# Performance work log

Hardware: AMD Instinct MI355X
Metric: run time of the kernel (lower is better)

Reference implementation:

```python
import jax, jax.numpy as jnp
import numpy as np

B, S, E = 4, 2048, 1024
H = 4
DH = E // H          # 256 head dim
DQ = E // 4          # 256 quaternion d_model
ALPHA = 1.5
EPS = 1e-10
FOCUS = 0.9
SEL = 2.0


def setup_inputs() -> dict:
    key = jax.random.key(0)
    ks = jax.random.split(key, 6)
    sc = 0.02
    return {
        "x": jax.random.normal(ks[0], (B, S, E), dtype=jnp.float32),
        "in_proj_w": jax.random.normal(ks[1], (3 * E, E), dtype=jnp.float32) * sc,
        "in_proj_b": jnp.zeros((3 * E,), dtype=jnp.float32),
        "out_w": jax.random.normal(ks[2], (E, E), dtype=jnp.float32) * sc,
        "out_b": jnp.zeros((E,), dtype=jnp.float32),
        "m_w1": jax.random.normal(ks[3], (E, E), dtype=jnp.float32) * sc,
        "m_b1": jnp.zeros((E,), dtype=jnp.float32),
        "m_w2": jax.random.normal(ks[4], (E, E), dtype=jnp.float32) * sc,
        "m_b2": jnp.zeros((E,), dtype=jnp.float32),
    }


def quaternion_multiply(q1, q2):
    # Hamilton product over last dim of size 4 (complex-valued components).
    w1, x1, y1, z1 = q1[..., 0], q1[..., 1], q1[..., 2], q1[..., 3]
    w2, x2, y2, z2 = q2[..., 0], q2[..., 1], q2[..., 2], q2[..., 3]
    return jnp.stack([
        w1 * w2 - x1 * x2 - y1 * y2 - z1 * z2,
        w1 * x2 + x1 * w2 + y1 * z2 - z1 * y2,
        w1 * y2 - x1 * z2 + y1 * w2 + z1 * x2,
        w1 * z2 + x1 * y2 - y1 * x2 + z1 * w2,
    ], axis=-1)


def _mha(x, in_proj_w, in_proj_b, out_w, out_b):
    # torch nn.MultiheadAttention self-attention, batch_first
    qkv = x @ in_proj_w.T + in_proj_b              # [B,S,3E]
    q, k, v = jnp.split(qkv, 3, axis=-1)
    q = q.reshape(B, S, H, DH)
    k = k.reshape(B, S, H, DH)
    v = v.reshape(B, S, H, DH)
    scores = jnp.einsum('bqhd,bkhd->bhqk', q, k) / jnp.sqrt(jnp.float32(DH))
    attn = jax.nn.softmax(scores, axis=-1)
    out = jnp.einsum('bhqk,bkhd->bqhd', attn, v).reshape(B, S, E)
    return out @ out_w.T + out_b


def _spectral_attention(signal):
    sq = signal.reshape(B, S, DQ, 4)
    sfft = jnp.fft.fft(sq, axis=-3)                 # complex64, FFT over seq
    kk = jnp.arange(S, dtype=jnp.float32)
    filt = jnp.exp(1j * ALPHA * jnp.arctan(jnp.log(kk + EPS)))  # [S] complex
    sf = sfft * filt[None, :, None, None]
    inter = quaternion_multiply(quaternion_multiply(sf, sf), sf)
    attended = jnp.fft.ifft(inter, axis=-3).real
    return attended.reshape(B, S, E)


def reference(x, in_proj_w, in_proj_b, out_w, out_b, m_w1, m_b1, m_w2, m_b2):
    nicotinic = _mha(x, in_proj_w, in_proj_b, out_w, out_b)
    h = jax.nn.gelu(x @ m_w1.T + m_b1, approximate=False)
    muscarinic = h @ m_w2.T + m_b2
    chol = FOCUS * nicotinic + (1.0 - FOCUS) * muscarinic
    attn_w = _spectral_attention(chol * SEL)
    return x * attn_w
```

## Files before the change

kernel.cpp:

```cpp
#include <hip/hip_runtime.h>
#include <cstdint>

typedef _Float16 f16;
typedef unsigned short u16;
typedef __attribute__((ext_vector_type(8))) _Float16 half8;
typedef __attribute__((ext_vector_type(4))) _Float16 half4;
typedef __attribute__((ext_vector_type(2))) __fp16 fp16x2;
typedef __attribute__((ext_vector_type(4))) float f32x4;

#define MFMA_F16(a, b, c) __builtin_amdgcn_mfma_f32_16x16x32_f16(a, b, c, 0, 0, 0)

#define WAITVM8() asm volatile("s_waitcnt vmcnt(8)" ::: "memory")
#define WAITVM4() asm volatile("s_waitcnt vmcnt(4)" ::: "memory")
#define WAITVM2() asm volatile("s_waitcnt vmcnt(2)" ::: "memory")
#define WAITVM0() asm volatile("s_waitcnt vmcnt(0)" ::: "memory")
#define BARRIER() do { asm volatile("" ::: "memory"); __builtin_amdgcn_s_barrier(); \
                       asm volatile("" ::: "memory"); } while (0)

__device__ inline void stage16(const void* g, void* l) {
#if defined(__has_builtin) && __has_builtin(__builtin_amdgcn_global_load_lds)
  __builtin_amdgcn_global_load_lds(
      (const __attribute__((address_space(1))) unsigned*)g,
      (__attribute__((address_space(3))) unsigned*)l, 16, 0, 0);
#else
  *(int4*)l = *(const int4*)g;
#endif
}

__device__ inline int pack_f16(float a, float b) {
#if defined(__has_builtin) && __has_builtin(__builtin_amdgcn_cvt_pkrtz)
  union { fp16x2 h; int i; } u;
  u.h = __builtin_amdgcn_cvt_pkrtz(a, b);
  return u.i;
#else
  union { f16 h[2]; int i; } u;
  u.h[0] = (f16)a; u.h[1] = (f16)b;
  return u.i;
#endif
}

__global__ __launch_bounds__(256)
void conv_all(const float* __restrict__ x, const float* __restrict__ wqkv,
              const float* __restrict__ w1, const float* __restrict__ wout,
              const float* __restrict__ w2, f16* __restrict__ dst) {
  int i = (blockIdx.x * 256 + threadIdx.x) * 8;
  const float* src; size_t dofs; float sc = 1.0f;
  if (i < 8388608)       { src = x + i;               dofs = i; }
  else if (i < 11534336) { src = wqkv + (i - 8388608); dofs = i; }
  else if (i < 12582912) { src = w1 + (i - 11534336);  dofs = i; }
  else if (i < 13631488) {
    int t = i - 12582912; int j = t >> 10, k = t & 1023;
    src = wout + t; dofs = 12582912 + (size_t)j * 2048 + k; sc = 1.8f;
  } else {
    int t = i - 13631488; int j = t >> 10, k = t & 1023;
    src = w2 + t; dofs = 12582912 + (size_t)j * 2048 + 1024 + k; sc = 0.2f;
  }
  float4 a = *(const float4*)src;
  float4 b = *(const float4*)(src + 4);
  half8 h;
  h[0] = (f16)(a.x * sc); h[1] = (f16)(a.y * sc); h[2] = (f16)(a.z * sc); h[3] = (f16)(a.w * sc);
  h[4] = (f16)(b.x * sc); h[5] = (f16)(b.y * sc); h[6] = (f16)(b.z * sc); h[7] = (f16)(b.w * sc);
  *(half8*)(dst + dofs) = h;
}

__global__ __launch_bounds__(256)
void filt_init(float2* __restrict__ ftab) {
  int k = blockIdx.x * 256 + threadIdx.x;
  if (k < 2048) {
    float s, c;
    sincosf(1.5f * atanf(logf((float)k + 1e-10f)), &s, &c);
    ftab[k] = make_float2(c, s);
  }
}

template<int EPI>
__global__ __launch_bounds__(256, 2)
void gemm_f16(const f16* __restrict__ A, const f16* __restrict__ W,
              const float* __restrict__ bias0, const float* __restrict__ bias1,
              void* __restrict__ out0, void* __restrict__ out1,
              f16* __restrict__ Vt, int N, int K) {
  __shared__ __align__(16) f16 lds[2][16384];
  const int tid = threadIdx.x;
  const int lane = tid & 63, w = tid >> 6;
  const int g = lane >> 4, lm = lane & 15;
  const int wr = w >> 1, wc = w & 1;
  const int nwg = gridDim.x * gridDim.y;
  const int flat = blockIdx.y * gridDim.x + blockIdx.x;
  const int logical = (flat & 7) * (nwg >> 3) + (flat >> 3);
  const int bx = logical % gridDim.x, by = logical / gridDim.x;
  const int m0 = by * 128, n0 = bx * 128;

  const f16* src[8];
#pragma unroll
  for (int j = 0; j < 8; ++j) {
    int u = j * 256 + tid;
    if (u < 1024) {
      int row = u >> 3, s = u & 7;
      src[j] = A + (size_t)(m0 + row) * K + ((s ^ (row & 7)) << 3);
    } else {
      int v = u - 1024;
      int row = v >> 3, s = v & 7;
      src[j] = W + (size_t)(n0 + row) * K + ((s ^ (row & 7)) << 3);
    }
  }

  f32x4 acc[4][4];
#pragma unroll
  for (int mt = 0; mt < 4; ++mt)
#pragma unroll
    for (int nt = 0; nt < 4; ++nt) acc[mt][nt] = (f32x4){0.f, 0.f, 0.f, 0.f};

#pragma unroll
  for (int j = 0; j < 8; ++j) stage16(src[j], &lds[0][(j * 256 + tid) * 8]);
  __syncthreads();

  const int KT = K >> 6;
#pragma unroll 1
  for (int t = 0; t < KT; ++t) {
    const f16* bufA = lds[t & 1];
    const f16* bufB = bufA + 8192;
    if (t + 1 < KT) {
#pragma unroll
      for (int j = 0; j < 8; ++j) {
        src[j] += 64;
        stage16(src[j], &lds[(t + 1) & 1][(j * 256 + tid) * 8]);
      }
      WAITVM8();
    } else {
      WAITVM0();
    }
    BARRIER();
#pragma unroll
    for (int ks = 0; ks < 2; ++ks) {
      half8 a[4], b[4];
#pragma unroll
      for (int mt = 0; mt < 4; ++mt) {
        int row = wr * 64 + mt * 16 + lm;
        a[mt] = *(const half8*)(bufA + row * 64 + (((ks * 4 + g) ^ (row & 7)) << 3));
      }
#pragma unroll
      for (int nt = 0; nt < 4; ++nt) {
        int row = wc * 64 + nt * 16 + lm;
        b[nt] = *(const half8*)(bufB + row * 64 + (((ks * 4 + g) ^ (row & 7)) << 3));
      }
#pragma unroll
      for (int mt = 0; mt < 4; ++mt)
#pragma unroll
        for (int nt = 0; nt < 4; ++nt)
          acc[mt][nt] = MFMA_F16(a[mt], b[nt], acc[mt][nt]);
    }
    BARRIER();
  }

  const int crow = m0 + wr * 64 + g * 4;
  const int ccol = n0 + wc * 64 + lm;
  if (EPI == 3) {
    if (n0 < 2048) {
      f16* qk = (f16*)out0;
#pragma unroll
      for (int nt = 0; nt < 4; ++nt) {
        float bb = bias0[ccol + nt * 16];
#pragma unroll
        for (int mt = 0; mt < 4; ++mt)
#pragma unroll
          for (int r = 0; r < 4; ++r)
            qk[(size_t)(crow + mt * 16 + r) * 3072 + ccol + nt * 16] =
                (f16)(acc[mt][nt][r] + bb);
      }
    } else if (n0 < 3072) {
      f16* ldsT = (f16*)lds;
#pragma unroll
      for (int nt = 0; nt < 4; ++nt) {
        float bb = bias0[ccol + nt * 16];
        int c = wc * 64 + nt * 16 + lm;
#pragma unroll
        for (int mt = 0; mt < 4; ++mt) {
          int r = wr * 64 + mt * 16 + g * 4;
#pragma unroll
          for (int rr = 0; rr < 4; ++rr)
            ldsT[c * 136 + r + rr] = (f16)(acc[mt][nt][rr] + bb);
        }
      }
      BARRIER();
      const int vbase0 = n0 - 2048;
      const int b = m0 >> 11, srow = m0 & 2047;
#pragma unroll
      for (int it = 0; it < 8; ++it) {
        int id = it * 256 + tid;
        int c = id >> 4, rb = id & 15;
        int vcol = vbase0 + c;
        int h = vcol >> 8, d = vcol & 255;
        half8 v = *(half8*)&ldsT[c * 136 + rb * 8];
        *(half8*)&Vt[(((size_t)(b * 4 + h)) * 256 + d) * 2048 + srow + rb * 8] = v;
      }
    } else {
      f16* cat = (f16*)out1;
      const int hc = ccol - 3072;
#pragma unroll
      for (int nt = 0; nt < 4; ++nt) {
        float bb = bias1[hc + nt * 16];
#pragma unroll
        for (int mt = 0; mt < 4; ++mt)
#pragma unroll
          for (int r = 0; r < 4; ++r) {
            float v = acc[mt][nt][r] + bb;
            v = 0.5f * v * (1.0f + erff(v * 0.70710678118654752f));
            cat[(size_t)(crow + mt * 16 + r) * 2048 + 1024 + hc + nt * 16] = (f16)v;
          }
      }
    }
  } else {
    f16* ldsT = (f16*)lds;
#pragma unroll
    for (int nt = 0; nt < 4; ++nt) {
      float bb = 1.8f * bias0[ccol + nt * 16] + 0.2f * bias1[ccol + nt * 16];
      int c = wc * 64 + nt * 16 + lm;
#pragma unroll
      for (int mt = 0; mt < 4; ++mt) {
        int r = wr * 64 + mt * 16 + g * 4;
#pragma unroll
        for (int rr = 0; rr < 4; ++rr)
          ldsT[c * 136 + r + rr] = (f16)(acc[mt][nt][rr] + bb);
      }
    }
    BARRIER();
    f16* ch = (f16*)out0;
#pragma unroll
    for (int it = 0; it < 8; ++it) {
      int id = it * 256 + tid;
      int c = id >> 4, rb = id & 15;
      half8 v = *(half8*)&ldsT[c * 136 + rb * 8];
      *(half8*)&ch[(size_t)(n0 + c) * 8192 + m0 + rb * 8] = v;
    }
  }
}

__global__ __launch_bounds__(512, 2)
void flash_f16(const f16* __restrict__ qkv, const f16* __restrict__ Vt,
               f16* __restrict__ attn) {
  __shared__ __align__(16) f16 lds[32768];
  const int tid = threadIdx.x;
  const int lane = tid & 63, w = tid >> 6;
  const int g = lane >> 4, lm = lane & 15;
  const int raw = blockIdx.x;
  const int bh = (raw & 7) * 2 + (raw >> 7);
  const int qt = (raw >> 3) & 15;
  const int b = bh >> 2, h = bh & 3;
  const int q0 = qt * 128 + w * 16;
  const float SC = 0.09016844005555896f;

  half8 qf[8];
  {
    const f16* qp = qkv + (size_t)(b * 2048 + q0 + lm) * 3072 + h * 256 + g * 8;
#pragma unroll
    for (int c = 0; c < 8; ++c) qf[c] = *(const half8*)(qp + c * 32);
  }

  const f16* kbase = qkv + (size_t)b * 2048 * 3072 + 1024 + h * 256;
  const f16* vbase = Vt + (size_t)bh * 256 * 2048;
  int kofs[2], vofs[2];
#pragma unroll
  for (int j = 0; j < 2; ++j) {
    int u = j * 512 + tid;
    int kv = u >> 5, s = u & 31;
    kofs[j] = kv * 3072 + ((s ^ (kv & 7)) << 3);
    int d = u >> 2, sl = u & 3;
    vofs[j] = d * 2048 + ((sl ^ ((d >> 1) & 3)) << 3);
  }

  f32x4 o[16];
#pragma unroll
  for (int f = 0; f < 16; ++f) o[f] = (f32x4){0.f, 0.f, 0.f, 0.f};
  float m = -3e38f, l = 0.f;
  half8 paP = (half8){0, 0, 0, 0, 0, 0, 0, 0};

#pragma unroll
  for (int j = 0; j < 2; ++j) stage16(kbase + kofs[j], &lds[(j * 512 + tid) * 8]);

#pragma unroll 1
  for (int t = 0; t < 64; ++t) {
    const int cb_ = t & 1;
    if (t < 63) {
      const int kt = (t + 1) * 98304;
#pragma unroll
      for (int j = 0; j < 2; ++j)
        stage16(kbase + kofs[j] + kt, &lds[(cb_ ^ 1) * 8192 + (j * 512 + tid) * 8]);
    }
    {
      const int vt_ = t * 32;
#pragma unroll
      for (int j = 0; j < 2; ++j)
        stage16(vbase + vofs[j] + vt_, &lds[16384 + cb_ * 8192 + (j * 512 + tid) * 8]);
    }
    if (t < 63) { WAITVM4(); } else { WAITVM2(); }
    BARRIER();

    const f16* kb = &lds[cb_ * 8192];

    f32x4 s0 = {0.f, 0.f, 0.f, 0.f}, s1 = {0.f, 0.f, 0.f, 0.f};
    __builtin_amdgcn_s_setprio(1);
#pragma unroll
    for (int c = 0; c < 8; ++c) {
      int slot = ((c * 4 + g) ^ (lm & 7)) << 3;
      half8 b0 = *(const half8*)(kb + lm * 256 + slot);
      half8 b1 = *(const half8*)(kb + (16 + lm) * 256 + slot);
      s0 = MFMA_F16(b0, qf[c], s0);
      s1 = MFMA_F16(b1, qf[c], s1);
    }
    __builtin_amdgcn_s_setprio(0);

    if (t > 0) {
      const f16* vbp = &lds[16384 + (cb_ ^ 1) * 8192];
      __builtin_amdgcn_s_setprio(1);
#pragma unroll
      for (int f = 0; f < 16; ++f) {
        int d = f * 16 + lm;
        half8 bv = *(const half8*)(vbp + d * 32 + ((g ^ ((d >> 1) & 3)) << 3));
        o[f] = MFMA_F16(paP, bv, o[f]);
      }
      __builtin_amdgcn_s_setprio(0);
    }

    float a0[4], a1[4];
#pragma unroll
    for (int r = 0; r < 4; ++r) { a0[r] = s0[r] * SC; a1[r] = s1[r] * SC; }
    float mx = fmaxf(fmaxf(fmaxf(a0[0], a0[1]), fmaxf(a0[2], a0[3])),
                     fmaxf(fmaxf(a1[0], a1[1]), fmaxf(a1[2], a1[3])));
    mx = fmaxf(mx, __shfl_xor(mx, 16));
    mx = fmaxf(mx, __shfl_xor(mx, 32));

    if (!__all(mx <= m + 8.0f)) {
      float mn = fmaxf(m, mx);
      float corr = exp2f(m - mn);
      m = mn; l *= corr;
#pragma unroll
      for (int r = 0; r < 4; ++r) {
        float cr = __shfl(corr, ((lane >> 2) & 12) + r);
#pragma unroll
        for (int f = 0; f < 16; ++f) o[f][r] *= cr;
      }
    }

    float e0[4], e1[4], rs;
#pragma unroll
    for (int r = 0; r < 4; ++r) { e0[r] = exp2f(a0[r] - m); e1[r] = exp2f(a1[r] - m); }
    rs = ((e0[0] + e0[1]) + (e0[2] + e0[3])) + ((e1[0] + e1[1]) + (e1[2] + e1[3]));
    rs += __shfl_xor(rs, 16);
    rs += __shfl_xor(rs, 32);
    l += rs;

    int A01 = pack_f16(e0[0], e0[1]);
    int A23 = pack_f16(e0[2], e0[3]);
    int B01 = pack_f16(e1[0], e1[1]);
    int B23 = pack_f16(e1[2], e1[3]);
    const int s1l = ((lane & 16) << 1) + lm;
    const int s2l = s1l + 16;
    int t0a = __shfl(A01, s1l), t0b = __shfl(B01, s1l);
    int t1a = __shfl(A23, s1l), t1b = __shfl(B23, s1l);
    int t2a = __shfl(A01, s2l), t2b = __shfl(B01, s2l);
    int t3a = __shfl(A23, s2l), t3b = __shfl(B23, s2l);
    union { int i[4]; half8 h; } pau;
    const bool hi = lane >= 32;
    pau.i[0] = hi ? t0b : t0a;
    pau.i[1] = hi ? t1b : t1a;
    pau.i[2] = hi ? t2b : t2a;
    pau.i[3] = hi ? t3b : t3a;
    paP = pau.h;

    BARRIER();
  }

  WAITVM0();
  BARRIER();
  {
    const f16* vbp = &lds[16384 + 8192];
#pragma unroll
    for (int f = 0; f < 16; ++f) {
      int d = f * 16 + lm;
      half8 bv = *(const half8*)(vbp + d * 32 + ((g ^ ((d >> 1) & 3)) << 3));
      o[f] = MFMA_F16(paP, bv, o[f]);
    }
  }

  float inv[4];
#pragma unroll
  for (int r = 0; r < 4; ++r) inv[r] = 1.0f / __shfl(l, ((lane >> 2) & 12) + r);
#pragma unroll
  for (int f = 0; f < 16; ++f)
#pragma unroll
    for (int r = 0; r < 4; ++r)
      attn[(size_t)(b * 2048 + q0 + g * 4 + r) * 2048 + h * 256 + f * 16 + lm] =
          (f16)(o[f][r] * inv[r]);
}

__device__ inline float2 cmul(float2 a, float2 b) {
  return make_float2(a.x * b.x - a.y * b.y, a.x * b.y + a.y * b.x);
}
__device__ inline float2 cmulc(float2 a, float2 b) {
  return make_float2(a.x * b.x + a.y * b.y, a.y * b.x - a.x * b.y);
}
__device__ inline void qcube(float2& w, float2& x, float2& y, float2& z, float2 f) {
  w = cmul(w, f); x = cmul(x, f); y = cmul(y, f); z = cmul(z, f);
  float2 a2 = cmul(w, w);
  float2 sx = cmul(x, x), sy = cmul(y, y), sz = cmul(z, z);
  float2 s = make_float2(sx.x + sy.x + sz.x, sx.y + sy.y + sz.y);
  float2 t3 = make_float2(a2.x - 3.f * s.x, a2.y - 3.f * s.y);
  float2 cf = make_float2(3.f * a2.x - s.x, 3.f * a2.y - s.y);
  w = cmul(w, t3); x = cmul(cf, x); y = cmul(cf, y); z = cmul(cf, z);
}

__device__ inline int fftpos(int k) {
  int kp = k >> 1;
  return ((k & 1) << 10) | ((kp & 3) << 8) | ((kp & 12) << 4) | (kp & 48)
       | ((kp >> 4) & 12) | ((kp >> 8) & 3);
}

__global__ __launch_bounds__(256)
void spectral6(const f16* __restrict__ cholT, const float* __restrict__ xin,
               const float2* __restrict__ ftab, float* __restrict__ outp) {
  __shared__ __align__(16) float2 Z[2][2048];
  __shared__ float2 tw[1024];
  const int tid = threadIdx.x;
  const int b = blockIdx.x >> 8;
  const int qd = blockIdx.x & 255;
  const size_t c0 = (size_t)qd * 4;
  const f16* t0 = cholT + (c0 + 0) * 8192 + b * 2048;
  const f16* t1 = cholT + (c0 + 1) * 8192 + b * 2048;
  const f16* t2 = cholT + (c0 + 2) * 8192 + b * 2048;
  const f16* t3 = cholT + (c0 + 3) * 8192 + b * 2048;

  for (int j = tid; j < 1024; j += 256) {
    float ang = -6.2831853071795864769f * (float)j * (1.0f / 2048.0f);
    float sv, cv; sincosf(ang, &sv, &cv);
    tw[j] = make_float2(cv, sv);
  }
  for (int s = tid; s < 1024; s += 256) {
    float2 z0a = make_float2((float)t0[s], (float)t1[s]);
    float2 z1a = make_float2((float)t2[s], (float)t3[s]);
    float2 z0b = make_float2((float)t0[s + 1024], (float)t1[s + 1024]);
    float2 z1b = make_float2((float)t2[s + 1024], (float)t3[s + 1024]);
    float2 w = tw[s];
    Z[0][s] = make_float2(z0a.x + z0b.x, z0a.y + z0b.y);
    Z[0][s + 1024] = cmul(make_float2(z0a.x - z0b.x, z0a.y - z0b.y), w);
    Z[1][s] = make_float2(z1a.x + z1b.x, z1a.y + z1b.y);
    Z[1][s + 1024] = cmul(make_float2(z1a.x - z1b.x, z1a.y - z1b.y), w);
  }
  __syncthreads();

#pragma unroll 1
  for (int lq = 8; lq >= 0; lq -= 2) {
    const int Q = 1 << lq, st = 512 >> lq;
#pragma unroll 1
    for (int it = 0; it < 4; ++it) {
      int gg = it * 256 + tid;
      int c = gg >> 9, bf = gg & 511;
      int j = bf & (Q - 1);
      int base = ((bf >> lq) << (lq + 2)) | j;
      float2 a = Z[c][base], bq = Z[c][base + Q];
      float2 cc = Z[c][base + 2 * Q], d = Z[c][base + 3 * Q];
      float2 t0_ = make_float2(a.x + cc.x, a.y + cc.y);
      float2 t1_ = make_float2(a.x - cc.x, a.y - cc.y);
      float2 t2_ = make_float2(bq.x + d.x, bq.y + d.y);
      float2 bd = make_float2(bq.x - d.x, bq.y - d.y);
      float2 t3_ = make_float2(bd.y, -bd.x);
      float2 y0 = make_float2(t0_.x + t2_.x, t0_.y + t2_.y);
      float2 y1 = make_float2(t1_.x + t3_.x, t1_.y + t3_.y);
      float2 y2 = make_float2(t0_.x - t2_.x, t0_.y - t2_.y);
      float2 y3 = make_float2(t1_.x - t3_.x, t1_.y - t3_.y);
      int i3 = 3 * j * st;
      float sg = (i3 & 1024) ? -1.f : 1.f;
      i3 &= 1023;
      Z[c][base] = y0;
      Z[c][base + Q] = cmul(y1, tw[j * st]);
      Z[c][base + 2 * Q] = cmul(y2, tw[2 * j * st]);
      float2 r3 = cmul(y3, tw[i3]);
      Z[c][base + 3 * Q] = make_float2(r3.x * sg, r3.y * sg);
    }
    __syncthreads();
  }

#pragma unroll 1
  for (int it = 0; it < 4; ++it) {
    int jj = it * 256 + tid;
    int nrep = (jj == 0) ? 2 : 1;
#pragma unroll 1
    for (int rep = 0; rep < nrep; ++rep) {
      int k  = (jj == 0) ? (rep ? 1024 : 0) : jj;
      int kn = (jj == 0) ? k : 2048 - jj;
      int p  = fftpos(k);
      int pp = fftpos(kn);
      float2 z0p = Z[0][p], z0q = Z[0][pp];
      float2 z1p = Z[1][p], z1q = Z[1][pp];
      float2 wk = make_float2(0.5f * (z0p.x + z0q.x), 0.5f * (z0p.y - z0q.y));
      float2 xk = make_float2(0.5f * (z0p.y + z0q.y), 0.5f * (z0q.x - z0p.x));
      float2 yk = make_float2(0.5f * (z1p.x + z1q.x), 0.5f * (z1p.y - z1q.y));
      float2 zk = make_float2(0.5f * (z1p.y + z1q.y), 0.5f * (z1q.x - z1p.x));
      float2 wn = make_float2(0.5f * (z0q.x + z0p.x), 0.5f * (z0q.y - z0p.y));
      float2 xn = make_float2(0.5f * (z0q.y + z0p.y), 0.5f * (z0p.x - z0q.x));
      float2 yn = make_float2(0.5f * (z1q.x + z1p.x), 0.5f * (z1q.y - z1p.y));
      float2 zn = make_float2(0.5f * (z1q.y + z1p.y), 0.5f * (z1p.x - z1q.x));
      float2 fk = ftab[k], fn = ftab[kn];
      qcube(wk, xk, yk, zk, fk);
      qcube(wn, xn, yn, zn, fn);
      Z[0][p]  = make_float2(0.5f * (wk.x + wn.x) - 0.5f * (xk.y - xn.y),
                             0.5f * (wk.y - wn.y) + 0.5f * (xk.x + xn.x));
      Z[0][pp] = make_float2(0.5f * (wn.x + wk.x) - 0.5f * (xn.y - xk.y),
                             0.5f * (wn.y - wk.y) + 0.5f * (xn.x + xk.x));
      Z[1][p]  = make_float2(0.5f * (yk.x + yn.x) - 0.5f * (zk.y - zn.y),
                             0.5f * (yk.y - yn.y) + 0.5f * (zk.x + zn.x));
      Z[1][pp] = make_float2(0.5f * (yn.x + yk.x) - 0.5f * (zn.y - zk.y),
                             0.5f * (yn.y - yk.y) + 0.5f * (zn.x + zk.x));
    }
  }
  __syncthreads();

#pragma unroll 1
  for (int lq = 0; lq <= 8; lq += 2) {
    const int Q = 1 << lq, st = 512 >> lq;
#pragma unroll 1
    for (int it = 0; it < 4; ++it) {
      int gg = it * 256 + tid;
      int c = gg >> 9, bf = gg & 511;
      int j = bf & (Q - 1);
      int base = ((bf >> lq) << (lq + 2)) | j;
      float2 a = Z[c][base];
      float2 bq = cmulc(Z[c][base + Q], tw[j * st]);
      float2 cc = cmulc(Z[c][base + 2 * Q], tw[2 * j * st]);
      int i3 = 3 * j * st;
      float sg = (i3 & 1024) ? -1.f : 1.f;
      i3 &= 1023;
      float2 d = cmulc(Z[c][base + 3 * Q], tw[i3]);
      d = make_float2(d.x * sg, d.y * sg);
      float2 t0_ = make_float2(a.x + cc.x, a.y + cc.y);
      float2 t1_ = make_float2(a.x - cc.x, a.y - cc.y);
      float2 t2_ = make_float2(bq.x + d.x, bq.y + d.y);
      float2 bd = make_float2(bq.x - d.x, bq.y - d.y);
      float2 t3_ = make_float2(-bd.y, bd.x);
      Z[c][base]         = make_float2(t0_.x + t2_.x, t0_.y + t2_.y);
      Z[c][base + Q]     = make_float2(t1_.x + t3_.x, t1_.y + t3_.y);
      Z[c][base + 2 * Q] = make_float2(t0_.x - t2_.x, t0_.y - t2_.y);
      Z[c][base + 3 * Q] = make_float2(t1_.x - t3_.x, t1_.y - t3_.y);
    }
    __syncthreads();
  }

  const float* xb = xin + (size_t)b * 2048 * 1024;
  float* ob = outp + (size_t)b * 2048 * 1024;
  const float inv = 1.0f / 2048.0f;
  for (int j = tid; j < 1024; j += 256) {
    float2 wj = tw[j];
    float2 a0 = Z[0][j], bw0 = cmulc(Z[0][j + 1024], wj);
    float2 a1 = Z[1][j], bw1 = cmulc(Z[1][j + 1024], wj);
    float2 r0lo = make_float2(a0.x + bw0.x, a0.y + bw0.y);
    float2 r0hi = make_float2(a0.x - bw0.x, a0.y - bw0.y);
    float2 r1lo = make_float2(a1.x + bw1.x, a1.y + bw1.y);
    float2 r1hi = make_float2(a1.x - bw1.x, a1.y - bw1.y);
    float4 xlo = *(const float4*)(xb + (size_t)j * 1024 + c0);
    float4 xhi = *(const float4*)(xb + (size_t)(j + 1024) * 1024 + c0);
    float4 olo, ohi;
    olo.x = xlo.x * r0lo.x * inv;
    olo.y = xlo.y * r0lo.y * inv;
    olo.z = xlo.z * r1lo.x * inv;
    olo.w = xlo.w * r1lo.y * inv;
    ohi.x = xhi.x * r0hi.x * inv;
    ohi.y = xhi.y * r0hi.y * inv;
    ohi.z = xhi.z * r1hi.x * inv;
    ohi.w = xhi.w * r1hi.y * inv;
    *(float4*)(ob + (size_t)j * 1024 + c0) = olo;
    *(float4*)(ob + (size_t)(j + 1024) * 1024 + c0) = ohi;
  }
}

extern "C" void kernel_launch(void* const* d_in, const int* in_sizes, int n_in,
                              void* d_out, int out_size, void* d_ws, size_t ws_size,
                              hipStream_t stream) {
  const float* x    = (const float*)d_in[0];
  const float* wqkv = (const float*)d_in[1];
  const float* bqkv = (const float*)d_in[2];
  const float* wout = (const float*)d_in[3];
  const float* bout = (const float*)d_in[4];
  const float* w1   = (const float*)d_in[5];
  const float* b1   = (const float*)d_in[6];
  const float* w2   = (const float*)d_in[7];
  const float* b2   = (const float*)d_in[8];
  float* out = (float*)d_out;
  char* wsb = (char*)d_ws;
  const size_t MB = 1048576;

  f16*   xf    = (f16*)(wsb);
  f16*   wqf   = (f16*)(wsb + 16 * MB);
  f16*   wcat  = (f16*)(wsb + 24 * MB);
  f16*   qkvF  = (f16*)(wsb + 32 * MB);
  f16*   VtF   = (f16*)(wsb + 80 * MB);
  f16*   cat   = (f16*)(wsb + 96 * MB);
  f16*   cholT = (f16*)(wsb + 128 * MB);
  float2* ftab = (float2*)(wsb + 145 * MB);

  filt_init<<<8, 256, 0, stream>>>(ftab);
  conv_all<<<7168, 256, 0, stream>>>(x, wqkv, w1, wout, w2, xf);

  gemm_f16<3><<<dim3(32, 64), 256, 0, stream>>>(xf, wqf, bqkv, b1, qkvF, cat, VtF, 4096, 1024);
  flash_f16<<<256, 512, 0, stream>>>(qkvF, VtF, cat);
  gemm_f16<4><<<dim3(8, 64), 256, 0, stream>>>(cat, wcat, bout, b2, cholT, nullptr, nullptr, 1024, 2048);
  spectral6<<<1024, 256, 0, stream>>>(cholT, x, ftab, out);
}
```

Baseline: 352.7 us.

## Double flash-attention KV tile, fold softmax scale into Q weights, precompute twiddles

The flash kernel now processes 64 keys per iteration instead of 32. It uses a larger double-buffered LDS region, a new V swizzle and two P fragments, which halves the number of loop iterations and barriers. The softmax scale is folded into the Q projection weights and bias during f16 conversion, so the per-score multiply disappears. The filter-table init is merged into the conversion kernel, which also precomputes FFT twiddles that the spectral kernel now reads instead of calling sincos. The cost is higher LDS use, occupancy limited to one flash block per CU, and a slight change in f16 rounding of Q.

After: 342.0 us (median of 2 runs). -3.0%, faster.

```diff
diff --git a/kernel.cpp b/kernel.cpp
--- a/kernel.cpp
+++ b/kernel.cpp
@@ -12,10 +12,11 @@
 
 #define WAITVM8() asm volatile("s_waitcnt vmcnt(8)" ::: "memory")
 #define WAITVM4() asm volatile("s_waitcnt vmcnt(4)" ::: "memory")
-#define WAITVM2() asm volatile("s_waitcnt vmcnt(2)" ::: "memory")
 #define WAITVM0() asm volatile("s_waitcnt vmcnt(0)" ::: "memory")
 #define BARRIER() do { asm volatile("" ::: "memory"); __builtin_amdgcn_s_barrier(); \
                        asm volatile("" ::: "memory"); } while (0)
+
+#define SCQ 0.09016844005555896f
 
 __device__ inline void stage16(const void* g, void* l) {
 #if defined(__has_builtin) && __has_builtin(__builtin_amdgcn_global_load_lds)
@@ -42,18 +43,37 @@
 __global__ __launch_bounds__(256)
 void conv_all(const float* __restrict__ x, const float* __restrict__ wqkv,
               const float* __restrict__ w1, const float* __restrict__ wout,
-              const float* __restrict__ w2, f16* __restrict__ dst) {
+              const float* __restrict__ w2, f16* __restrict__ dst,
+              float2* __restrict__ tab) {
+  if (blockIdx.x >= 7168) {
+    int kk = (blockIdx.x - 7168) * 256 + threadIdx.x;
+    if (kk < 2048) {
+      float s, c;
+      sincosf(1.5f * atanf(logf((float)kk + 1e-10f)), &s, &c);
+      tab[kk] = make_float2(c, s);
+    } else if (kk < 3072) {
+      int j = kk - 2048;
+      float s, c;
+      sincosf(-6.2831853071795864769f * (float)j * (1.0f / 2048.0f), &s, &c);
+      tab[kk] = make_float2(c, s);
+    }
+    return;
+  }
   int i = (blockIdx.x * 256 + threadIdx.x) * 8;
   const float* src; size_t dofs; float sc = 1.0f;
   if (i < 8388608)       { src = x + i;               dofs = i; }
-  else if (i < 11534336) { src = wqkv + (i - 8388608); dofs = i; }
+  else if (i < 11534336) {
+    int t = i - 8388608;
+    src = wqkv + t; dofs = i;
+    if ((t >> 10) < 1024) sc = SCQ;
+  }
   else if (i < 12582912) { src = w1 + (i - 11534336);  dofs = i; }
   else if (i < 13631488) {
     int t = i - 12582912; int j = t >> 10, k = t & 1023;
     src = wout + t; dofs = 12582912 + (size_t)j * 2048 + k; sc = 1.8f;
   } else {
     int t = i - 13631488; int j = t >> 10, k = t & 1023;
-    src = w2 + t; dofs = 12582912 + (size_t)j * 2048 + 1024 + k; sc = 0.2f;
+    src = w2 + t; dofs = 13631488 - 1048576 + (size_t)j * 2048 + 1024 + k; sc = 0.2f;
   }
   float4 a = *(const float4*)src;
   float4 b = *(const float4*)(src + 4);
@@ -61,16 +81,6 @@
   h[0] = (f16)(a.x * sc); h[1] = (f16)(a.y * sc); h[2] = (f16)(a.z * sc); h[3] = (f16)(a.w * sc);
   h[4] = (f16)(b.x * sc); h[5] = (f16)(b.y * sc); h[6] = (f16)(b.z * sc); h[7] = (f16)(b.w * sc);
   *(half8*)(dst + dofs) = h;
-}
-
-__global__ __launch_bounds__(256)
-void filt_init(float2* __restrict__ ftab) {
-  int k = blockIdx.x * 256 + threadIdx.x;
-  if (k < 2048) {
-    float s, c;
-    sincosf(1.5f * atanf(logf((float)k + 1e-10f)), &s, &c);
-    ftab[k] = make_float2(c, s);
-  }
 }
 
 template<int EPI>
@@ -157,9 +167,10 @@
   if (EPI == 3) {
     if (n0 < 2048) {
       f16* qk = (f16*)out0;
+      const float bsc = (n0 < 1024) ? SCQ : 1.0f;
 #pragma unroll
       for (int nt = 0; nt < 4; ++nt) {
-        float bb = bias0[ccol + nt * 16];
+        float bb = bias0[ccol + nt * 16] * bsc;
 #pragma unroll
         for (int mt = 0; mt < 4; ++mt)
 #pragma unroll
@@ -235,10 +246,10 @@
   }
 }
 
-__global__ __launch_bounds__(512, 2)
+__global__ __launch_bounds__(512, 1)
 void flash_f16(const f16* __restrict__ qkv, const f16* __restrict__ Vt,
                f16* __restrict__ attn) {
-  __shared__ __align__(16) f16 lds[32768];
+  __shared__ __align__(16) f16 lds[65536];
   const int tid = threadIdx.x;
   const int lane = tid & 63, w = tid >> 6;
   const int g = lane >> 4, lm = lane & 15;
@@ -247,7 +258,6 @@
   const int qt = (raw >> 3) & 15;
   const int b = bh >> 2, h = bh & 3;
   const int q0 = qt * 128 + w * 16;
-  const float SC = 0.09016844005555896f;
 
   half8 qf[8];
   {
@@ -258,74 +268,83 @@
 
   const f16* kbase = qkv + (size_t)b * 2048 * 3072 + 1024 + h * 256;
   const f16* vbase = Vt + (size_t)bh * 256 * 2048;
-  int kofs[2], vofs[2];
-#pragma unroll
-  for (int j = 0; j < 2; ++j) {
+  int kofs[4], vofs[4];
+#pragma unroll
+  for (int j = 0; j < 4; ++j) {
     int u = j * 512 + tid;
     int kv = u >> 5, s = u & 31;
     kofs[j] = kv * 3072 + ((s ^ (kv & 7)) << 3);
-    int d = u >> 2, sl = u & 3;
-    vofs[j] = d * 2048 + ((sl ^ ((d >> 1) & 3)) << 3);
+    int d = u >> 3, sl = u & 7;
+    vofs[j] = d * 2048 + ((sl ^ (d & 7)) << 3);
   }
 
   f32x4 o[16];
 #pragma unroll
   for (int f = 0; f < 16; ++f) o[f] = (f32x4){0.f, 0.f, 0.f, 0.f};
   float m = -3e38f, l = 0.f;
-  half8 paP = (half8){0, 0, 0, 0, 0, 0, 0, 0};
-
-#pragma unroll
-  for (int j = 0; j < 2; ++j) stage16(kbase + kofs[j], &lds[(j * 512 + tid) * 8]);
-
-#pragma unroll 1
-  for (int t = 0; t < 64; ++t) {
+  half8 paP0 = (half8){0, 0, 0, 0, 0, 0, 0, 0};
+  half8 paP1 = (half8){0, 0, 0, 0, 0, 0, 0, 0};
+
+#pragma unroll
+  for (int j = 0; j < 4; ++j) stage16(kbase + kofs[j], &lds[(j * 512 + tid) * 8]);
+
+#pragma unroll 1
+  for (int t = 0; t < 32; ++t) {
     const int cb_ = t & 1;
-    if (t < 63) {
-      const int kt = (t + 1) * 98304;
-#pragma unroll
-      for (int j = 0; j < 2; ++j)
-        stage16(kbase + kofs[j] + kt, &lds[(cb_ ^ 1) * 8192 + (j * 512 + tid) * 8]);
+    if (t < 31) {
+      const int kt = (t + 1) * 196608;
+#pragma unroll
+      for (int j = 0; j < 4; ++j)
+        stage16(kbase + kofs[j] + kt, &lds[(cb_ ^ 1) * 16384 + (j * 512 + tid) * 8]);
     }
     {
-      const int vt_ = t * 32;
-#pragma unroll
-      for (int j = 0; j < 2; ++j)
-        stage16(vbase + vofs[j] + vt_, &lds[16384 + cb_ * 8192 + (j * 512 + tid) * 8]);
-    }
-    if (t < 63) { WAITVM4(); } else { WAITVM2(); }
+      const int vt_ = t * 64;
+#pragma unroll
+      for (int j = 0; j < 4; ++j)
+        stage16(vbase + vofs[j] + vt_, &lds[32768 + cb_ * 16384 + (j * 512 + tid) * 8]);
+    }
+    if (t < 31) { WAITVM8(); } else { WAITVM4(); }
     BARRIER();
 
-    const f16* kb = &lds[cb_ * 8192];
+    const f16* kb = &lds[cb_ * 16384];
 
     f32x4 s0 = {0.f, 0.f, 0.f, 0.f}, s1 = {0.f, 0.f, 0.f, 0.f};
+    f32x4 s2 = {0.f, 0.f, 0.f, 0.f}, s3 = {0.f, 0.f, 0.f, 0.f};
     __builtin_amdgcn_s_setprio(1);
 #pragma unroll
     for (int c = 0; c < 8; ++c) {
       int slot = ((c * 4 + g) ^ (lm & 7)) << 3;
-      half8 b0 = *(const half8*)(kb + lm * 256 + slot);
-      half8 b1 = *(const half8*)(kb + (16 + lm) * 256 + slot);
+      const f16* kr = kb + lm * 256 + slot;
+      half8 b0 = *(const half8*)(kr);
+      half8 b1 = *(const half8*)(kr + 16 * 256);
+      half8 b2 = *(const half8*)(kr + 32 * 256);
+      half8 b3 = *(const half8*)(kr + 48 * 256);
       s0 = MFMA_F16(b0, qf[c], s0);
       s1 = MFMA_F16(b1, qf[c], s1);
+      s2 = MFMA_F16(b2, qf[c], s2);
+      s3 = MFMA_F16(b3, qf[c], s3);
     }
     __builtin_amdgcn_s_setprio(0);
 
     if (t > 0) {
-      const f16* vbp = &lds[16384 + (cb_ ^ 1) * 8192];
+      const f16* vbp = &lds[32768 + (cb_ ^ 1) * 16384];
       __builtin_amdgcn_s_setprio(1);
 #pragma unroll
       for (int f = 0; f < 16; ++f) {
         int d = f * 16 + lm;
-        half8 bv = *(const half8*)(vbp + d * 32 + ((g ^ ((d >> 1) & 3)) << 3));
-        o[f] = MFMA_F16(paP, bv, o[f]);
+        const f16* vr = vbp + d * 64;
+        half8 bv0 = *(const half8*)(vr + ((g ^ (d & 7)) << 3));
+        half8 bv1 = *(const half8*)(vr + (((4 + g) ^ (d & 7)) << 3));
+        o[f] = MFMA_F16(paP0, bv0, o[f]);
+        o[f] = MFMA_F16(paP1, bv1, o[f]);
       }
       __builtin_amdgcn_s_setprio(0);
     }
 
-    float a0[4], a1[4];
-#pragma unroll
-    for (int r = 0; r < 4; ++r) { a0[r] = s0[r] * SC; a1[r] = s1[r] * SC; }
-    float mx = fmaxf(fmaxf(fmaxf(a0[0], a0[1]), fmaxf(a0[2], a0[3])),
-                     fmaxf(fmaxf(a1[0], a1[1]), fmaxf(a1[2], a1[3])));
+    float mx = fmaxf(fmaxf(fmaxf(s0[0], s0[1]), fmaxf(s0[2], s0[3])),
+                     fmaxf(fmaxf(s1[0], s1[1]), fmaxf(s1[2], s1[3])));
+    mx = fmaxf(mx, fmaxf(fmaxf(fmaxf(s2[0], s2[1]), fmaxf(s2[2], s2[3])),
+                         fmaxf(fmaxf(s3[0], s3[1]), fmaxf(s3[2], s3[3]))));
     mx = fmaxf(mx, __shfl_xor(mx, 16));
     mx = fmaxf(mx, __shfl_xor(mx, 32));
 
@@ -341,31 +360,55 @@
       }
     }
 
-    float e0[4], e1[4], rs;
-#pragma unroll
-    for (int r = 0; r < 4; ++r) { e0[r] = exp2f(a0[r] - m); e1[r] = exp2f(a1[r] - m); }
-    rs = ((e0[0] + e0[1]) + (e0[2] + e0[3])) + ((e1[0] + e1[1]) + (e1[2] + e1[3]));
+    float e0[4], e1[4], e2[4], e3[4];
+#pragma unroll
+    for (int r = 0; r < 4; ++r) {
+      e0[r] = exp2f(s0[r] - m);
+      e1[r] = exp2f(s1[r] - m);
+      e2[r] = exp2f(s2[r] - m);
+      e3[r] = exp2f(s3[r] - m);
+    }
+    float rs = ((e0[0] + e0[1]) + (e0[2] + e0[3])) + ((e1[0] + e1[1]) + (e1[2] + e1[3]))
+             + ((e2[0] + e2[1]) + (e2[2] + e2[3])) + ((e3[0] + e3[1]) + (e3[2] + e3[3]));
     rs += __shfl_xor(rs, 16);
     rs += __shfl_xor(rs, 32);
     l += rs;
 
-    int A01 = pack_f16(e0[0], e0[1]);
-    int A23 = pack_f16(e0[2], e0[3]);
-    int B01 = pack_f16(e1[0], e1[1]);
-    int B23 = pack_f16(e1[2], e1[3]);
     const int s1l = ((lane & 16) << 1) + lm;
     const int s2l = s1l + 16;
-    int t0a = __shfl(A01, s1l), t0b = __shfl(B01, s1l);
-    int t1a = __shfl(A23, s1l), t1b = __shfl(B23, s1l);
-    int t2a = __shfl(A01, s2l), t2b = __shfl(B01, s2l);
-    int t3a = __shfl(A23, s2l), t3b = __shfl(B23, s2l);
-    union { int i[4]; half8 h; } pau;
     const bool hi = lane >= 32;
-    pau.i[0] = hi ? t0b : t0a;
-    pau.i[1] = hi ? t1b : t1a;
-    pau.i[2] = hi ? t2b : t2a;
-    pau.i[3] = hi ? t3b : t3a;
-    paP = pau.h;
+    {
+      int A01 = pack_f16(e0[0], e0[1]);
+      int A23 = pack_f16(e0[2], e0[3]);
+      int B01 = pack_f16(e1[0], e1[1]);
+      int B23 = pack_f16(e1[2], e1[3]);
+      int t0a = __shfl(A01, s1l), t0b = __shfl(B01, s1l);
+      int t1a = __shfl(A23, s1l), t1b = __shfl(B23, s1l);
+      int t2a = __shfl(A01, s2l), t2b = __shfl(B01, s2l);
+      int t3a = __shfl(A23, s2l), t3b = __shfl(B23, s2l);
+      union { int i[4]; half8 h; } pau;
+      pau.i[0] = hi ? t0b : t0a;
+      pau.i[1] = hi ? t1b : t1a;
+      pau.i[2] = hi ? t2b : t2a;
+      pau.i[3] = hi ? t3b : t3a;
+      paP0 = pau.h;
+    }
+    {
+      int A01 = pack_f16(e2[0], e2[1]);
+      int A23 = pack_f16(e2[2], e2[3]);
+      int B01 = pack_f16(e3[0], e3[1]);
+      int B23 = pack_f16(e3[2], e3[3]);
+      int t0a = __shfl(A01, s1l), t0b = __shfl(B01, s1l);
+      int t1a = __shfl(A23, s1l), t1b = __shfl(B23, s1l);
+      int t2a = __shfl(A01, s2l), t2b = __shfl(B01, s2l);
+      int t3a = __shfl(A23, s2l), t3b = __shfl(B23, s2l);
+      union { int i[4]; half8 h; } pau;
+      pau.i[0] = hi ? t0b : t0a;
+      pau.i[1] = hi ? t1b : t1a;
+      pau.i[2] = hi ? t2b : t2a;
+      pau.i[3] = hi ? t3b : t3a;
+      paP1 = pau.h;
+    }
 
     BARRIER();
   }
@@ -373,12 +416,15 @@
   WAITVM0();
   BARRIER();
   {
-    const f16* vbp = &lds[16384 + 8192];
+    const f16* vbp = &lds[32768 + 16384];
 #pragma unroll
     for (int f = 0; f < 16; ++f) {
       int d = f * 16 + lm;
-      half8 bv = *(const half8*)(vbp + d * 32 + ((g ^ ((d >> 1) & 3)) << 3));
-      o[f] = MFMA_F16(paP, bv, o[f]);
+      const f16* vr = vbp + d * 64;
+      half8 bv0 = *(const half8*)(vr + ((g ^ (d & 7)) << 3));
+      half8 bv1 = *(const half8*)(vr + (((4 + g) ^ (d & 7)) << 3));
+      o[f] = MFMA_F16(paP0, bv0, o[f]);
+      o[f] = MFMA_F16(paP1, bv1, o[f]);
     }
   }
 
@@ -416,8 +462,8 @@
 }
 
 __global__ __launch_bounds__(256)
-void spectral6(const f16* __restrict__ cholT, const float* __restrict__ xin,
-               const float2* __restrict__ ftab, float* __restrict__ outp) {
+void spectral7(const f16* __restrict__ cholT, const float* __restrict__ xin,
+               const float2* __restrict__ tab, float* __restrict__ outp) {
   __shared__ __align__(16) float2 Z[2][2048];
   __shared__ float2 tw[1024];
   const int tid = threadIdx.x;
@@ -428,18 +474,16 @@
   const f16* t1 = cholT + (c0 + 1) * 8192 + b * 2048;
   const f16* t2 = cholT + (c0 + 2) * 8192 + b * 2048;
   const f16* t3 = cholT + (c0 + 3) * 8192 + b * 2048;
-
-  for (int j = tid; j < 1024; j += 256) {
-    float ang = -6.2831853071795864769f * (float)j * (1.0f / 2048.0f);
-    float sv, cv; sincosf(ang, &sv, &cv);
-    tw[j] = make_float2(cv, sv);
-  }
+  const float2* ftab = tab;
+  const float2* twt = tab + 2048;
+
+  for (int j = tid; j < 1024; j += 256) tw[j] = twt[j];
   for (int s = tid; s < 1024; s += 256) {
     float2 z0a = make_float2((float)t0[s], (float)t1[s]);
     float2 z1a = make_float2((float)t2[s], (float)t3[s]);
     float2 z0b = make_float2((float)t0[s + 1024], (float)t1[s + 1024]);
     float2 z1b = make_float2((float)t2[s + 1024], (float)t3[s + 1024]);
-    float2 w = tw[s];
+    float2 w = twt[s];
     Z[0][s] = make_float2(z0a.x + z0b.x, z0a.y + z0b.y);
     Z[0][s + 1024] = cmul(make_float2(z0a.x - z0b.x, z0a.y - z0b.y), w);
     Z[1][s] = make_float2(z1a.x + z1b.x, z1a.y + z1b.y);
@@ -594,13 +638,12 @@
   f16*   VtF   = (f16*)(wsb + 80 * MB);
   f16*   cat   = (f16*)(wsb + 96 * MB);
   f16*   cholT = (f16*)(wsb + 128 * MB);
-  float2* ftab = (float2*)(wsb + 145 * MB);
-
-  filt_init<<<8, 256, 0, stream>>>(ftab);
-  conv_all<<<7168, 256, 0, stream>>>(x, wqkv, w1, wout, w2, xf);
+  float2* tab  = (float2*)(wsb + 145 * MB);
+
+  conv_all<<<7184, 256, 0, stream>>>(x, wqkv, w1, wout, w2, xf, tab);
 
   gemm_f16<3><<<dim3(32, 64), 256, 0, stream>>>(xf, wqf, bqkv, b1, qkvF, cat, VtF, 4096, 1024);
   flash_f16<<<256, 512, 0, stream>>>(qkvF, VtF, cat);
   gemm_f16<4><<<dim3(8, 64), 256, 0, stream>>>(cat, wcat, bout, b2, cholT, nullptr, nullptr, 1024, 2048);
-  spectral6<<<1024, 256, 0, stream>>>(cholT, x, ftab, out);
-}
+  spectral7<<<1024, 256, 0, stream>>>(cholT, x, tab, out);
+}
```
